# Kernel tuning notes

Measured on AMD Instinct MI355X. Metric: run time of the kernel, lower is better.

## Reference

```python
import jax, jax.numpy as jnp
import numpy as np

VOCAB, EMBED, SEQ, HID = 50000, 128, 200, 30
BATCH = 4096


def setup_inputs() -> dict:
    key = jax.random.key(0)
    ks = jax.random.split(key, 14)
    s = lambda fan_in: 1.0 / np.sqrt(fan_in)
    return {
        "tokens": jax.random.randint(ks[0], (BATCH, SEQ), 0, VOCAB, dtype=jnp.int32),
        "emb": jax.random.normal(ks[1], (VOCAB, EMBED), jnp.float32) * 0.05,
        "Wx": jax.random.normal(ks[2], (EMBED, HID), jnp.float32) * s(EMBED),
        "Wh": jax.random.normal(ks[3], (HID, HID), jnp.float32) * s(HID),
        "b_rnn": jnp.zeros((HID,), jnp.float32),
        "W1": jax.random.normal(ks[4], (HID, 128), jnp.float32) * s(HID),
        "b1": jnp.zeros((128,), jnp.float32),
        "W2": jax.random.normal(ks[5], (128, 64), jnp.float32) * s(128),
        "b2": jnp.zeros((64,), jnp.float32),
        "W3": jax.random.normal(ks[6], (64, 32), jnp.float32) * s(64),
        "b3": jnp.zeros((32,), jnp.float32),
        "Wo": jax.random.normal(ks[7], (32, 1), jnp.float32) * s(32),
        "bo": jnp.zeros((1,), jnp.float32),
    }


def reference(tokens, emb, Wx, Wh, b_rnn, W1, b1, W2, b2, W3, b3, Wo, bo):
    # Embedding lookup: [B, T, E]
    x = emb[tokens]
    # SimpleRNN (tanh), return last hidden state. Precompute input projection
    # once as a big GEMM, then scan the recurrence over time.
    xp = jnp.einsum("bte,eh->tbh", x, Wx) + b_rnn  # [T, B, H]
    h0 = jnp.zeros((tokens.shape[0], Wh.shape[0]), x.dtype)

    def step(h, xp_t):
        h_new = jnp.tanh(xp_t + h @ Wh)
        return h_new, None

    h_last, _ = jax.lax.scan(step, h0, xp)
    # Dense head (dropout layers are identity at inference).
    d1 = jax.nn.relu(h_last @ W1 + b1)
    d2 = jax.nn.relu(d1 @ W2 + b2)
    d3 = jax.nn.relu(d2 @ W3 + b3)
    return jax.nn.sigmoid(d3 @ Wo + bo)
```

## Files before the change

kernel.cpp:

```cpp
#include <hip/hip_runtime.h>
#include <math.h>

#define VOCAB 50000
#define EMBED 128
#define SEQ   200
#define HID   30
#define BATCH 4096

typedef float4 __attribute__((__may_alias__)) f4ma;

__device__ __forceinline__ float tanh_fast(float x) {
    float e = __expf(2.0f * x);
    return 1.0f - __fdividef(2.0f, e + 1.0f);
}

__global__ __launch_bounds__(256) void embproj_kernel(
    const float* __restrict__ emb, const float* __restrict__ Wx,
    const float* __restrict__ brnn, float* __restrict__ embP)
{
    __shared__ float WxL[EMBED * HID];
    __shared__ float bL[32];
    int tid = threadIdx.x;
    for (int i = tid; i < EMBED * HID; i += 256) WxL[i] = Wx[i];
    if (tid < HID) bL[tid] = brnn[tid];
    __syncthreads();

    int g  = tid >> 5;
    int j  = tid & 31;
    int jj = (j < HID) ? j : 0;
    int v0 = blockIdx.x * 32 + g * 4;

    int vr0 = min(v0 + 0, VOCAB - 1);
    int vr1 = min(v0 + 1, VOCAB - 1);
    int vr2 = min(v0 + 2, VOCAB - 1);
    int vr3 = min(v0 + 3, VOCAB - 1);
    const float4* e0 = (const float4*)(emb + (size_t)vr0 * EMBED);
    const float4* e1 = (const float4*)(emb + (size_t)vr1 * EMBED);
    const float4* e2 = (const float4*)(emb + (size_t)vr2 * EMBED);
    const float4* e3 = (const float4*)(emb + (size_t)vr3 * EMBED);

    float bj = (j < HID) ? bL[jj] : 0.0f;
    float acc[4][4];
    #pragma unroll
    for (int rr = 0; rr < 4; ++rr) {
        acc[rr][0] = bj; acc[rr][1] = 0.f; acc[rr][2] = 0.f; acc[rr][3] = 0.f;
    }

    #pragma unroll 4
    for (int q = 0; q < EMBED / 4; ++q) {
        float4 r0 = e0[q], r1 = e1[q], r2 = e2[q], r3 = e3[q];
        #pragma unroll
        for (int d = 0; d < 4; ++d) {
            float w = WxL[(4 * q + d) * HID + jj];
            acc[0][d] += (&r0.x)[d] * w;
            acc[1][d] += (&r1.x)[d] * w;
            acc[2][d] += (&r2.x)[d] * w;
            acc[3][d] += (&r3.x)[d] * w;
        }
    }
    if (j < HID) {
        #pragma unroll
        for (int rr = 0; rr < 4; ++rr) {
            if (v0 + rr < VOCAB)
                embP[(size_t)(v0 + rr) * HID + j] =
                    (acc[rr][0] + acc[rr][1]) + (acc[rr][2] + acc[rr][3]);
        }
    }
}

__global__ __launch_bounds__(256, 2) void rnn_head_kernel(
    const int* __restrict__ tokens, const float* __restrict__ embP,
    const float* __restrict__ Wh,
    const float* __restrict__ W1, const float* __restrict__ b1,
    const float* __restrict__ W2, const float* __restrict__ b2,
    const float* __restrict__ W3, const float* __restrict__ b3,
    const float* __restrict__ Wo, const float* __restrict__ bo,
    float* __restrict__ out)
{
    __shared__ __align__(16) float hL[8][36];
    __shared__ float d1L[8][128];
    __shared__ float d2L[8][64];

    int tid  = threadIdx.x;
    int wv   = tid >> 6;
    int l    = tid & 63;
    int half = l >> 5;
    int j    = l & 31;
    int rloc = wv * 2 + half;
    int b    = blockIdx.x * 8 + rloc;

    const int* trow = tokens + (size_t)b * SEQ;
    int jc = (j < HID) ? j : (HID - 1);

    hL[rloc][j] = 0.0f;
    __builtin_amdgcn_sched_barrier(0);

    float whc[32];
    #pragma unroll
    for (int k = 0; k < 32; ++k)
        whc[k] = (k < HID && j < HID) ? Wh[k * HID + j] : 0.0f;

    float xq[8];
    int   tr[8];
    #pragma unroll
    for (int s = 0; s < 8; ++s) {
        xq[s] = embP[(size_t)trow[s] * HID + jc];
        tr[s] = trow[8 + s];
    }

    for (int t = 0; t < SEQ; t += 8) {
        #pragma unroll
        for (int s = 0; s < 8; ++s) {
            float hv[32];
            const f4ma* h4 = (const f4ma*)(&hL[rloc][0]);
            #pragma unroll
            for (int qq = 0; qq < 8; ++qq) {
                f4ma hh = h4[qq];
                hv[4*qq+0] = hh.x; hv[4*qq+1] = hh.y;
                hv[4*qq+2] = hh.z; hv[4*qq+3] = hh.w;
            }
            float a0 = xq[s], a1 = 0.0f, a2 = 0.0f, a3 = 0.0f;
            xq[s] = embP[(size_t)tr[s] * HID + jc];
            int tn = t + 16 + s; tn = (tn < SEQ) ? tn : SEQ - 1;
            tr[s] = trow[tn];

            #pragma unroll
            for (int k = 0; k < 32; k += 4) {
                a0 += hv[k]     * whc[k];
                a1 += hv[k + 1] * whc[k + 1];
                a2 += hv[k + 2] * whc[k + 2];
                a3 += hv[k + 3] * whc[k + 3];
            }
            float hn = tanh_fast((a0 + a1) + (a2 + a3));
            if (j < HID) hL[rloc][j] = hn;
            __builtin_amdgcn_sched_barrier(0);
        }
    }

    {
        #pragma unroll
        for (int qq = 0; qq < 4; ++qq) {
            int c = j + 32 * qq;
            float acc = b1[c];
            #pragma unroll
            for (int k = 0; k < HID; ++k) acc += hL[rloc][k] * W1[k * 128 + c];
            d1L[rloc][c] = fmaxf(acc, 0.0f);
        }
        #pragma unroll
        for (int qq = 0; qq < 2; ++qq) {
            int c = j + 32 * qq;
            float acc = b2[c];
            #pragma unroll 8
            for (int k = 0; k < 128; ++k) acc += d1L[rloc][k] * W2[k * 64 + c];
            d2L[rloc][c] = fmaxf(acc, 0.0f);
        }
        float acc3 = b3[j];
        #pragma unroll 8
        for (int k = 0; k < 64; ++k) acc3 += d2L[rloc][k] * W3[k * 32 + j];
        acc3 = fmaxf(acc3, 0.0f);
        float prod = acc3 * Wo[j];
        #pragma unroll
        for (int m = 16; m > 0; m >>= 1) prod += __shfl_xor(prod, m, 32);
        if (j == 0) out[b] = 1.0f / (1.0f + __expf(-(prod + bo[0])));
    }
}

extern "C" void kernel_launch(void* const* d_in, const int* in_sizes, int n_in,
                              void* d_out, int out_size, void* d_ws, size_t ws_size,
                              hipStream_t stream) {
    (void)in_sizes; (void)n_in; (void)out_size; (void)ws_size;
    const int*   tokens = (const int*)  d_in[0];
    const float* emb    = (const float*)d_in[1];
    const float* Wx     = (const float*)d_in[2];
    const float* Wh     = (const float*)d_in[3];
    const float* brnn   = (const float*)d_in[4];
    const float* W1     = (const float*)d_in[5];
    const float* b1     = (const float*)d_in[6];
    const float* W2     = (const float*)d_in[7];
    const float* b2     = (const float*)d_in[8];
    const float* W3     = (const float*)d_in[9];
    const float* b3     = (const float*)d_in[10];
    const float* Wo     = (const float*)d_in[11];
    const float* bo     = (const float*)d_in[12];
    float* out  = (float*)d_out;
    float* embP = (float*)d_ws;

    embproj_kernel<<<(VOCAB + 31) / 32, 256, 0, stream>>>(emb, Wx, brnn, embP);
    rnn_head_kernel<<<BATCH / 8, 256, 0, stream>>>(
        tokens, embP, Wh, W1, b1, W2, b2, W3, b3, Wo, bo, out);
}
```

Measured before the change: 107.0 us.

## Split-K across half-waves with ds_swizzle in projection and recurrence kernels

The embedding-projection kernel is rewritten so each lane keeps 64 Wx weights in registers instead of staging Wx in shared memory. Each lane handles half of the embed dimension, vocab rows are streamed with a double-buffered load, and partial sums are combined with a ds_swizzle across 16 lanes. In the RNN step, each lane now reads only 16 hidden values from LDS and computes partials for two output columns, exchanging one via swizzle. This cuts LDS read width and shortens the dot-product chain, at the cost of an extra cross-lane op on the serial recurrence path and higher register pressure.

```diff
diff --git a/kernel.cpp b/kernel.cpp
--- a/kernel.cpp
+++ b/kernel.cpp
@@ -13,59 +13,63 @@
     float e = __expf(2.0f * x);
     return 1.0f - __fdividef(2.0f, e + 1.0f);
 }
-
-__global__ __launch_bounds__(256) void embproj_kernel(
+__device__ __forceinline__ float swz16_f(float x) {
+    return __int_as_float(__builtin_amdgcn_ds_swizzle(__float_as_int(x), 0x401F));
+}
+
+__global__ __launch_bounds__(256, 2) void embproj_kernel(
     const float* __restrict__ emb, const float* __restrict__ Wx,
     const float* __restrict__ brnn, float* __restrict__ embP)
 {
-    __shared__ float WxL[EMBED * HID];
-    __shared__ float bL[32];
-    int tid = threadIdx.x;
-    for (int i = tid; i < EMBED * HID; i += 256) WxL[i] = Wx[i];
-    if (tid < HID) bL[tid] = brnn[tid];
-    __syncthreads();
-
-    int g  = tid >> 5;
-    int j  = tid & 31;
-    int jj = (j < HID) ? j : 0;
-    int v0 = blockIdx.x * 32 + g * 4;
-
-    int vr0 = min(v0 + 0, VOCAB - 1);
-    int vr1 = min(v0 + 1, VOCAB - 1);
-    int vr2 = min(v0 + 2, VOCAB - 1);
-    int vr3 = min(v0 + 3, VOCAB - 1);
-    const float4* e0 = (const float4*)(emb + (size_t)vr0 * EMBED);
-    const float4* e1 = (const float4*)(emb + (size_t)vr1 * EMBED);
-    const float4* e2 = (const float4*)(emb + (size_t)vr2 * EMBED);
-    const float4* e3 = (const float4*)(emb + (size_t)vr3 * EMBED);
-
-    float bj = (j < HID) ? bL[jj] : 0.0f;
-    float acc[4][4];
+    int tid  = threadIdx.x;
+    int wv   = tid >> 6;
+    int l    = tid & 63;
+    int j16  = l & 15;
+    int p    = (l >> 4) & 1;
+    int g    = l >> 5;
+    int col  = j16 + 16 * g;
+    int colc = (col < HID) ? col : (HID - 1);
+    int k0   = 64 * p;
+
+    float whx[64];
     #pragma unroll
-    for (int rr = 0; rr < 4; ++rr) {
-        acc[rr][0] = bj; acc[rr][1] = 0.f; acc[rr][2] = 0.f; acc[rr][3] = 0.f;
-    }
-
-    #pragma unroll 4
-    for (int q = 0; q < EMBED / 4; ++q) {
-        float4 r0 = e0[q], r1 = e1[q], r2 = e2[q], r3 = e3[q];
-        #pragma unroll
-        for (int d = 0; d < 4; ++d) {
-            float w = WxL[(4 * q + d) * HID + jj];
-            acc[0][d] += (&r0.x)[d] * w;
-            acc[1][d] += (&r1.x)[d] * w;
-            acc[2][d] += (&r2.x)[d] * w;
-            acc[3][d] += (&r3.x)[d] * w;
-        }
-    }
-    if (j < HID) {
-        #pragma unroll
-        for (int rr = 0; rr < 4; ++rr) {
-            if (v0 + rr < VOCAB)
-                embP[(size_t)(v0 + rr) * HID + j] =
-                    (acc[rr][0] + acc[rr][1]) + (acc[rr][2] + acc[rr][3]);
-        }
-    }
+    for (int i = 0; i < 64; ++i)
+        whx[i] = Wx[(k0 + i) * HID + colc];
+    float bj = brnn[colc];
+
+    int base = (blockIdx.x * 4 + wv) * 25;
+
+    float4 eA[16], eB[16];
+    #define LOADROW(dst, v) { \
+        int vc = min((v), VOCAB - 1); \
+        const f4ma* e4 = (const f4ma*)(emb + (size_t)vc * EMBED + k0); \
+        _Pragma("unroll") \
+        for (int q = 0; q < 16; ++q) dst[q] = e4[q]; \
+    }
+    #define COMPUTE(src, v) { \
+        float a0 = 0.f, a1 = 0.f, a2 = 0.f, a3 = 0.f; \
+        _Pragma("unroll") \
+        for (int q = 0; q < 16; ++q) { \
+            a0 += src[q].x * whx[4*q+0]; \
+            a1 += src[q].y * whx[4*q+1]; \
+            a2 += src[q].z * whx[4*q+2]; \
+            a3 += src[q].w * whx[4*q+3]; \
+        } \
+        float own  = (a0 + a1) + (a2 + a3); \
+        float full = bj + (own + swz16_f(own)); \
+        if (p == 0 && col < HID && (v) < VOCAB) \
+            embP[(size_t)(v) * HID + col] = full; \
+    }
+
+    LOADROW(eA, base + 0);
+    for (int r = 0; r < 25; r += 2) {
+        LOADROW(eB, base + r + 1);
+        COMPUTE(eA, base + r);
+        LOADROW(eA, base + r + 2);
+        COMPUTE(eB, base + r + 1);
+    }
+    #undef LOADROW
+    #undef COMPUTE
 }
 
 __global__ __launch_bounds__(256, 2) void rnn_head_kernel(
@@ -77,7 +81,7 @@
     const float* __restrict__ Wo, const float* __restrict__ bo,
     float* __restrict__ out)
 {
-    __shared__ __align__(16) float hL[8][36];
+    __shared__ __align__(16) float hL[8][32];
     __shared__ float d1L[8][128];
     __shared__ float d2L[8][64];
 
@@ -86,6 +90,8 @@
     int l    = tid & 63;
     int half = l >> 5;
     int j    = l & 31;
+    int j16  = l & 15;
+    int p    = (l >> 4) & 1;
     int rloc = wv * 2 + half;
     int b    = blockIdx.x * 8 + rloc;
 
@@ -95,13 +101,16 @@
     hL[rloc][j] = 0.0f;
     __builtin_amdgcn_sched_barrier(0);
 
-    float whc[32];
+    int cB = j16 + 16;
+    float whA[16], whB[16];
     #pragma unroll
-    for (int k = 0; k < 32; ++k)
-        whc[k] = (k < HID && j < HID) ? Wh[k * HID + j] : 0.0f;
-
-    float xq[8];
-    int   tr[8];
+    for (int kk = 0; kk < 16; ++kk) {
+        int k = 16 * p + kk;
+        whA[kk] = (k < HID) ? Wh[k * HID + j16] : 0.0f;
+        whB[kk] = (k < HID && cB < HID) ? Wh[k * HID + cB] : 0.0f;
+    }
+
+    float xq[8]; int tr[8];
     #pragma unroll
     for (int s = 0; s < 8; ++s) {
         xq[s] = embP[(size_t)trow[s] * HID + jc];
@@ -111,27 +120,33 @@
     for (int t = 0; t < SEQ; t += 8) {
         #pragma unroll
         for (int s = 0; s < 8; ++s) {
-            float hv[32];
-            const f4ma* h4 = (const f4ma*)(&hL[rloc][0]);
+            float hv[16];
+            const f4ma* h4 = (const f4ma*)(&hL[rloc][16 * p]);
             #pragma unroll
-            for (int qq = 0; qq < 8; ++qq) {
+            for (int qq = 0; qq < 4; ++qq) {
                 f4ma hh = h4[qq];
                 hv[4*qq+0] = hh.x; hv[4*qq+1] = hh.y;
                 hv[4*qq+2] = hh.z; hv[4*qq+3] = hh.w;
             }
-            float a0 = xq[s], a1 = 0.0f, a2 = 0.0f, a3 = 0.0f;
+            float xp = xq[s];
             xq[s] = embP[(size_t)tr[s] * HID + jc];
             int tn = t + 16 + s; tn = (tn < SEQ) ? tn : SEQ - 1;
             tr[s] = trow[tn];
 
+            float a0=0.f, a1=0.f, b0=0.f, b1=0.f;
             #pragma unroll
-            for (int k = 0; k < 32; k += 4) {
-                a0 += hv[k]     * whc[k];
-                a1 += hv[k + 1] * whc[k + 1];
-                a2 += hv[k + 2] * whc[k + 2];
-                a3 += hv[k + 3] * whc[k + 3];
+            for (int kk = 0; kk < 16; kk += 2) {
+                a0 += hv[kk]   * whA[kk];
+                a1 += hv[kk+1] * whA[kk+1];
+                b0 += hv[kk]   * whB[kk];
+                b1 += hv[kk+1] * whB[kk+1];
             }
-            float hn = tanh_fast((a0 + a1) + (a2 + a3));
+            float pA = a0 + a1;
+            float pB = b0 + b1;
+            float own  = p ? pB : pA;
+            float send = p ? pA : pB;
+            float recv = swz16_f(send);
+            float hn = tanh_fast(xp + (own + recv));
             if (j < HID) hL[rloc][j] = hn;
             __builtin_amdgcn_sched_barrier(0);
         }
@@ -185,7 +200,7 @@
     float* out  = (float*)d_out;
     float* embP = (float*)d_ws;
 
-    embproj_kernel<<<(VOCAB + 31) / 32, 256, 0, stream>>>(emb, Wx, brnn, embP);
+    embproj_kernel<<<512, 256, 0, stream>>>(emb, Wx, brnn, embP);
     rnn_head_kernel<<<BATCH / 8, 256, 0, stream>>>(
         tokens, embP, Wh, W1, b1, W2, b2, W3, b3, Wo, bo, out);
 }
```

After: 95.56 us. 10.7% less time.
